# Optimization experiments

Hardware: AMD Instinct MI355X
Metric: run time of the kernel (lower is better)

Reference implementation:

```python
import jax, jax.numpy as jnp
import numpy as np

N, E, B = 200000, 1600000, 4096
IN_FEATS, H, R, NB = 64, 32, 8, 2


def _params(key):
    ks = jax.random.split(key, 20)
    p = {}
    dims = [(IN_FEATS, H), (H, H), (H, H), (H, H)]
    i = 0
    for l, (di, do) in enumerate(dims):
        p[f'basis{l}'] = jax.random.normal(ks[i], (NB, di, do), jnp.float32) * 0.1; i += 1
        p[f'comp{l}'] = jax.random.normal(ks[i], (R, NB), jnp.float32) * 0.1; i += 1
        p[f'wself{l}'] = jax.random.normal(ks[i], (di, do), jnp.float32) * 0.1; i += 1
        p[f'bias{l}'] = jnp.zeros((do,), jnp.float32); i += 1
    p['lin1_w'] = jax.random.normal(ks[i], (2 * 4 * H, 1), jnp.float32) * 0.05; i += 1
    p['lin1_b'] = jnp.zeros((1,), jnp.float32)
    return p


def setup_inputs() -> dict:
    key = jax.random.key(0)
    k = jax.random.split(key, 8)
    inp = {
        'x': jax.random.normal(k[0], (N, IN_FEATS), jnp.float32),
        'src': jax.random.randint(k[1], (E,), 0, N, jnp.int32),
        'dst': jax.random.randint(k[2], (E,), 0, N, jnp.int32),
        'etype': jax.random.randint(k[3], (E,), 0, R, jnp.int32),
        'user_idx': jax.random.randint(k[4], (B,), 0, N, jnp.int32),
        'item_idx': jax.random.randint(k[5], (B,), 0, N, jnp.int32),
    }
    inp.update(_params(k[6]))
    return inp


def _rel_graph_conv(x, src, dst, etype, basis, comp, wself, bias):
    # basis decomposition: W_r = sum_b comp[r,b] * basis[b]
    # compute per-node per-basis transform first (cheap: small NB), then mix per edge
    hb = jnp.einsum('ni,bio->nbo', x, basis)            # [N, NB, out]
    msg = jnp.einsum('eb,ebo->eo', comp[etype], hb[src])  # [E, out]
    agg = jax.ops.segment_sum(msg, dst, num_segments=x.shape[0])
    return agg + x @ wself + bias


def reference(x, src, dst, etype, user_idx, item_idx,
              basis0, comp0, wself0, bias0,
              basis1, comp1, wself1, bias1,
              basis2, comp2, wself2, bias2,
              basis3, comp3, wself3, bias3,
              lin1_w, lin1_b):
    states = []
    h = x
    for (ba, co, ws, bi) in ((basis0, comp0, wself0, bias0),
                             (basis1, comp1, wself1, bias1),
                             (basis2, comp2, wself2, bias2),
                             (basis3, comp3, wself3, bias3)):
        h = jnp.tanh(_rel_graph_conv(h, src, dst, etype, ba, co, ws, bi))
        states.append(h)
    cat = jnp.concatenate(states, axis=1)               # [N, 128]
    pair = jnp.concatenate([cat[user_idx], cat[item_idx]], axis=1)  # [B, 256]
    out = jax.nn.sigmoid(pair @ lin1_w + lin1_b)        # [B, 1]
    return out[:, 0]  # multiply_by == 1
```

## Files before the change

kernel.cpp:

```cpp
#include <hip/hip_runtime.h>
#include <hip/hip_bf16.h>


#define SRC_MASK 0x3FFFFu
#define BUK_SH 9
#define BUK_W 512

typedef __attribute__((ext_vector_type(8))) short bf16x8;
typedef __attribute__((ext_vector_type(4))) float f32x4;

__device__ inline unsigned int f2bf(float f) {
    unsigned int u = __float_as_uint(f);
    return (u + 0x7FFFu + ((u >> 16) & 1u)) >> 16;
}

__device__ inline float fast_tanh(float x) {
    float xc = fminf(fmaxf(x, -15.f), 15.f);
    float e = __expf(2.f * xc);
    return (e - 1.f) * __builtin_amdgcn_rcpf(e + 1.f);
}

__device__ inline void block_exscan(int* a, int M, int* wsum ) {
    const int t = threadIdx.x;
    const int q = M >> 2;
    int s0 = 0, s1 = 0, s2 = 0, s3 = 0, s = 0;
    if (t < q) {
        s0 = a[4 * t]; s1 = a[4 * t + 1]; s2 = a[4 * t + 2]; s3 = a[4 * t + 3];
        s = s0 + s1 + s2 + s3;
    }
    int lane = t & 63, wid = t >> 6;
    int val = s;
    for (int d = 1; d < 64; d <<= 1) {
        int u = __shfl_up(val, d, 64);
        if (lane >= d) val += u;
    }
    if (lane == 63) wsum[wid] = val;
    __syncthreads();
    int woff = 0;
    for (int w = 0; w < wid; ++w) woff += wsum[w];
    val += woff;
    int base = val - s;
    __syncthreads();
    if (t < q) {
        a[4 * t]     = base;
        a[4 * t + 1] = base + s0;
        a[4 * t + 2] = base + s0 + s1;
        a[4 * t + 3] = base + s0 + s1 + s2;
    }
    __syncthreads();
}

__global__ __launch_bounds__(256) void k_buk_count(const int* __restrict__ dst,
                                                   int* __restrict__ gBukCnt, int E) {
    __shared__ int hist[1024];
    const int t = threadIdx.x;
    for (int f = t; f < 1024; f += 256) hist[f] = 0;
    __syncthreads();
    int e0 = blockIdx.x * 2048;
    for (int k = 0; k < 8; ++k) {
        int e = e0 + k * 256 + t;
        if (e < E) atomicAdd(&hist[dst[e] >> BUK_SH], 1);
    }
    __syncthreads();
    for (int f = t; f < 1024; f += 256) {
        int c = hist[f];
        if (c) atomicAdd(&gBukCnt[f], c);
    }
}

__global__ void k_buk_scan(const int* __restrict__ gBukCnt, int* __restrict__ bukOff,
                           int nb) {
    __shared__ int lds[1024];
    int tid = threadIdx.x;
    int v = (tid < nb) ? gBukCnt[tid] : 0;
    lds[tid] = v;
    __syncthreads();
    for (int d = 1; d < 1024; d <<= 1) {
        int u = (tid >= d) ? lds[tid - d] : 0;
        __syncthreads();
        lds[tid] += u;
        __syncthreads();
    }
    if (tid < nb) bukOff[tid] = lds[tid] - v;
    if (tid == nb - 1) bukOff[nb] = lds[tid];
}

__global__ __launch_bounds__(256) void k_binscatter(
    const int* __restrict__ src, const int* __restrict__ dst,
    const int* __restrict__ etype, const int* __restrict__ bukOff,
    int* __restrict__ gBukCur, unsigned int* __restrict__ binned,
    int E, int NBUK)
{
    __shared__ int hist[1024];
    __shared__ int offs[1024];
    __shared__ int cur[1024];
    __shared__ int gb[1024];
    __shared__ int wsum[4];
    __shared__ unsigned int stage[2048];
    __shared__ unsigned short stageB[2048];
    const int t = threadIdx.x;
    for (int f = t; f < 1024; f += 256) { hist[f] = 0; cur[f] = 0; }
    __syncthreads();

    const int e0 = blockIdx.x * 2048;
    const int cntTot = min(2048, E - e0);
    unsigned int pk[8];
    int bk[8];
#pragma unroll
    for (int k = 0; k < 8; ++k) {
        int e = e0 + k * 256 + t;
        if (e < E) {
            int d = dst[e];
            bk[k] = d >> BUK_SH;
            pk[k] = (unsigned int)src[e]
                  | ((unsigned int)etype[e] << 29)
                  | ((unsigned int)(d & (BUK_W - 1)) << 20);
            atomicAdd(&hist[bk[k]], 1);
        } else bk[k] = -1;
    }
    __syncthreads();
    for (int f = t; f < 1024; f += 256) offs[f] = hist[f];
    __syncthreads();
    block_exscan(offs, 1024, wsum);
#pragma unroll
    for (int k = 0; k < 8; ++k) {
        if (bk[k] >= 0) {
            int pos = offs[bk[k]] + atomicAdd(&cur[bk[k]], 1);
            stage[pos] = pk[k];
            stageB[pos] = (unsigned short)bk[k];
        }
    }
    for (int f = t; f < NBUK; f += 256) {
        int c = hist[f];
        if (c > 0) gb[f] = bukOff[f] + atomicAdd(&gBukCur[f], c);
    }
    __syncthreads();
    for (int k = t; k < cntTot; k += 256) {
        int b = stageB[k];
        binned[(size_t)gb[b] + (size_t)(k - offs[b])] = stage[k];
    }
}

__global__ __launch_bounds__(256) void k_bucket_finalize(
    const unsigned int* __restrict__ binned, const int* __restrict__ bukOff,
    int* __restrict__ rowptr, unsigned int* __restrict__ epack, int N, int E)
{
    __shared__ int nhist[512];
    __shared__ int ncur[512];
    __shared__ int wsum[4];
    const int t = threadIdx.x;
    const int b = blockIdx.x;
    for (int f = t; f < 512; f += 256) { nhist[f] = 0; ncur[f] = 0; }
    __syncthreads();
    const int k0 = bukOff[b], k1 = bukOff[b + 1];
    for (int k = k0 + t; k < k1; k += 256)
        atomicAdd(&nhist[(binned[k] >> 20) & (BUK_W - 1)], 1);
    __syncthreads();
    block_exscan(nhist, 512, wsum);
    for (int f = t; f < 512; f += 256) {
        int node = (b << BUK_SH) + f;
        if (node < N) rowptr[node] = k0 + nhist[f];
    }
    if (b == 0 && t == 0) rowptr[N] = E;
    for (int k = k0 + t; k < k1; k += 256) {
        unsigned int v = binned[k];
        int dl = (v >> 20) & (BUK_W - 1);
        int pos = k0 + nhist[dl] + atomicAdd(&ncur[dl], 1);
        epack[pos] = v & 0xE003FFFFu;
    }
}

template<int DI>
__global__ __launch_bounds__(256) void k_transform3(
    const float* __restrict__ xin, int in_stride,
    const float* __restrict__ basis, const float* __restrict__ wself,
    const float* __restrict__ bias,
    unsigned int* __restrict__ hb2, float* __restrict__ selfout, int n)
{
    constexpr int ROWB = DI * 2;
    constexpr int SMASK = (ROWB / 16) - 1;
    constexpr int C4 = DI / 4;
    __shared__ unsigned short xs[64 * DI];
    __shared__ unsigned short bt[96 * DI];
    const int t = threadIdx.x;

    auto swz = [](int row, int byteInRow) -> int {
        int slot = (byteInRow >> 4) ^ ((row ^ (row >> 2)) & SMASK);
        return row * ROWB + (slot << 4) + (byteInRow & 15);
    };

    for (int f = t; f < 96 * C4; f += 256) {
        int k4 = f / 96;
        int o  = f - k4 * 96;
        const float* sp = (o < 64) ? (basis + (size_t)(o >> 5) * DI * 32 + (o & 31))
                                   : (wself + (o - 64));
        int k = 4 * k4;
        ushort4 pv;
        pv.x = (unsigned short)f2bf(sp[(size_t)(k + 0) * 32]);
        pv.y = (unsigned short)f2bf(sp[(size_t)(k + 1) * 32]);
        pv.z = (unsigned short)f2bf(sp[(size_t)(k + 2) * 32]);
        pv.w = (unsigned short)f2bf(sp[(size_t)(k + 3) * 32]);
        *(ushort4*)((char*)bt + swz(o, k * 2)) = pv;
    }

    const int node0 = blockIdx.x * 64;
    for (int f = t; f < 64 * C4; f += 256) {
        int nloc = f / C4, k4 = f - nloc * C4;
        int node = node0 + nloc;
        float4 v = make_float4(0.f, 0.f, 0.f, 0.f);
        if (node < n) v = *(const float4*)(xin + (size_t)node * in_stride + 4 * k4);
        ushort4 pv;
        pv.x = (unsigned short)f2bf(v.x);
        pv.y = (unsigned short)f2bf(v.y);
        pv.z = (unsigned short)f2bf(v.z);
        pv.w = (unsigned short)f2bf(v.w);
        *(ushort4*)((char*)xs + swz(nloc, 8 * k4)) = pv;
    }
    __syncthreads();

    const int w = t >> 6;
    const int l = t & 63;
    const int lr = l & 15;
    const int lg = l >> 4;

    f32x4 c[6];
#pragma unroll
    for (int i = 0; i < 6; ++i) c[i] = (f32x4){0.f, 0.f, 0.f, 0.f};

#pragma unroll
    for (int ks = 0; ks < DI / 32; ++ks) {
        const int kb = ks * 64 + lg * 16;
        bf16x8 a = *(const bf16x8*)((char*)xs + swz(w * 16 + lr, kb));
#pragma unroll
        for (int tt = 0; tt < 6; ++tt) {
            bf16x8 b = *(const bf16x8*)((char*)bt + swz(tt * 16 + lr, kb));
            c[tt] = __builtin_amdgcn_mfma_f32_16x16x32_bf16(a, b, c[tt], 0, 0, 0);
        }
    }

    const float bia0 = bias[lr];
    const float bia1 = bias[16 + lr];
#pragma unroll
    for (int r = 0; r < 4; ++r) {
        int node = node0 + w * 16 + lg * 4 + r;
        if (node < n) {
            hb2[(size_t)node * 32 + lr]      = f2bf(c[0][r]) | (f2bf(c[2][r]) << 16);
            hb2[(size_t)node * 32 + 16 + lr] = f2bf(c[1][r]) | (f2bf(c[3][r]) << 16);
            selfout[(size_t)node * 128 + lr]      = c[4][r] + bia0;
            selfout[(size_t)node * 128 + 16 + lr] = c[5][r] + bia1;
        }
    }
}

__global__ __launch_bounds__(256) void k_aggregate(
    const unsigned int* __restrict__ hb2,
    const unsigned int* __restrict__ epack,
    const int* __restrict__ rowptr,
    const float* __restrict__ comp,
    float* __restrict__ cat_l,
    int n)
{
    __shared__ unsigned int cw[8];
    if (threadIdx.x < 8)
        cw[threadIdx.x] = f2bf(comp[threadIdx.x * 2 + 0])
                        | (f2bf(comp[threadIdx.x * 2 + 1]) << 16);
    __syncthreads();
    int t = blockIdx.x * 256 + threadIdx.x;
    int node = t >> 3;
    int oj = t & 7;
    if (node >= n) return;
    float* cp = cat_l + (size_t)node * 128 + 4 * oj;
    float4 acc = *(float4*)cp;
    const int k0 = rowptr[node], k1 = rowptr[node + 1];
    const unsigned gbase = (unsigned)oj * 16u;
    for (int k = k0; k < k1; k += 8) {
        unsigned int pp[8];
        uint4 hh[8];
#pragma unroll
        for (int j = 0; j < 8; ++j)
            pp[j] = epack[min(k + j, k1 - 1)];
#pragma unroll
        for (int j = 0; j < 8; ++j) {
            unsigned boff = (pp[j] & SRC_MASK) * 128u + gbase;
            hh[j] = *(const uint4*)((const char*)hb2 + boff);
        }
#pragma unroll
        for (int j = 0; j < 8; ++j) {
            bool valid = (k + j) < k1;
            unsigned w = cw[pp[j] >> 29];
            float w0 = __uint_as_float(w << 16);
            float w1 = __uint_as_float(w & 0xFFFF0000u);
            unsigned hx = valid ? hh[j].x : 0u;
            unsigned hy = valid ? hh[j].y : 0u;
            unsigned hz = valid ? hh[j].z : 0u;
            unsigned hw = valid ? hh[j].w : 0u;
            acc.x = fmaf(w0, __uint_as_float(hx << 16), acc.x);
            acc.x = fmaf(w1, __uint_as_float(hx & 0xFFFF0000u), acc.x);
            acc.y = fmaf(w0, __uint_as_float(hy << 16), acc.y);
            acc.y = fmaf(w1, __uint_as_float(hy & 0xFFFF0000u), acc.y);
            acc.z = fmaf(w0, __uint_as_float(hz << 16), acc.z);
            acc.z = fmaf(w1, __uint_as_float(hz & 0xFFFF0000u), acc.z);
            acc.w = fmaf(w0, __uint_as_float(hw << 16), acc.w);
            acc.w = fmaf(w1, __uint_as_float(hw & 0xFFFF0000u), acc.w);
        }
    }
    float4 r;
    r.x = fast_tanh(acc.x);
    r.y = fast_tanh(acc.y);
    r.z = fast_tanh(acc.z);
    r.w = fast_tanh(acc.w);
    *(float4*)cp = r;
}

__global__ void k_head(const float* __restrict__ cat, const int* __restrict__ uidx,
                       const int* __restrict__ iidx, const float* __restrict__ w,
                       const float* __restrict__ b, float* __restrict__ out, int B) {
    int p = blockIdx.x;
    if (p >= B) return;
    int lane = threadIdx.x;
    const float* cu = cat + (size_t)uidx[p] * 128;
    const float* ci = cat + (size_t)iidx[p] * 128;
    float s = 0.f;
    s = fmaf(cu[lane], w[lane], s);
    s = fmaf(cu[lane + 64], w[lane + 64], s);
    s = fmaf(ci[lane], w[lane + 128], s);
    s = fmaf(ci[lane + 64], w[lane + 192], s);
    for (int d = 32; d > 0; d >>= 1) s += __shfl_down(s, d, 64);
    if (lane == 0) out[p] = 1.f / (1.f + expf(-(s + b[0])));
}

extern "C" void kernel_launch(void* const* d_in, const int* in_sizes, int n_in,
                              void* d_out, int out_size, void* d_ws, size_t ws_size,
                              hipStream_t stream) {
    const float* x      = (const float*)d_in[0];
    const int*   src    = (const int*)d_in[1];
    const int*   dst    = (const int*)d_in[2];
    const int*   etype  = (const int*)d_in[3];
    const int*   uidx   = (const int*)d_in[4];
    const int*   iidx   = (const int*)d_in[5];
    const float* lin1_w = (const float*)d_in[22];
    const float* lin1_b = (const float*)d_in[23];

    const int N = in_sizes[0] / 64;
    const int E = in_sizes[1];
    const int B = in_sizes[4];
    const int NBUK = (N + BUK_W - 1) >> BUK_SH;

    char* p = (char*)d_ws;
    auto alloc = [&](size_t bytes) -> void* {
        void* r = (void*)p;
        p += (bytes + 255) & ~(size_t)255;
        return r;
    };
    unsigned int* hb2     = (unsigned int*)alloc((size_t)N * 32 * sizeof(unsigned int));
    float*        cat     = (float*)alloc((size_t)N * 128 * sizeof(float));
    int*          rowptr  = (int*)alloc((size_t)(N + 1) * sizeof(int));
    unsigned int* epack   = (unsigned int*)alloc((size_t)E * sizeof(unsigned int));
    unsigned int* binned  = (unsigned int*)alloc((size_t)E * sizeof(unsigned int));
    int*          gBukCnt = (int*)alloc(1024 * sizeof(int));
    int*          gBukCur = (int*)alloc(1024 * sizeof(int));
    int*          bukOff  = (int*)alloc(1025 * sizeof(int));

    hipMemsetAsync(gBukCnt, 0, 2048 * sizeof(int), stream);
    int ebGrid = (E + 2047) / 2048;
    k_buk_count<<<ebGrid, 256, 0, stream>>>(dst, gBukCnt, E);
    k_buk_scan<<<1, 1024, 0, stream>>>(gBukCnt, bukOff, NBUK);
    k_binscatter<<<ebGrid, 256, 0, stream>>>(src, dst, etype, bukOff, gBukCur,
                                             binned, E, NBUK);
    k_bucket_finalize<<<NBUK, 256, 0, stream>>>(binned, bukOff, rowptr, epack, N, E);

    int tr_grid = (N + 63) / 64;
    int agg_grid = (N * 8 + 255) / 256;
    for (int l = 0; l < 4; ++l) {
        const float* xin   = (l == 0) ? x : (cat + (size_t)(l - 1) * 32);
        int in_stride      = (l == 0) ? 64 : 128;
        const float* basis = (const float*)d_in[6 + l * 4];
        const float* comp  = (const float*)d_in[7 + l * 4];
        const float* wself = (const float*)d_in[8 + l * 4];
        const float* bias  = (const float*)d_in[9 + l * 4];
        if (l == 0)
            k_transform3<64><<<tr_grid, 256, 0, stream>>>(xin, in_stride, basis, wself,
                                                          bias, hb2, cat + (size_t)l * 32, N);
        else
            k_transform3<32><<<tr_grid, 256, 0, stream>>>(xin, in_stride, basis, wself,
                                                          bias, hb2, cat + (size_t)l * 32, N);
        k_aggregate<<<agg_grid, 256, 0, stream>>>(hb2, epack, rowptr, comp,
                                                  cat + (size_t)l * 32, N);
    }

    k_head<<<B, 64, 0, stream>>>(cat, uidx, iidx, lin1_w, lin1_b, (float*)d_out, B);
}
```

Measured before the change: 291.6 us.

## Sort nodes by in-degree to balance aggregate wavefront work

Adds a counting sort of nodes by in-degree (histogram, scan, scatter kernels) and has the aggregate kernel process nodes in that order. Nodes in the same wavefront then have similar edge counts, which cuts divergence in the per-node edge loop. The cost is three extra kernels per call, one more level of indirection, and scattered rather than sequential writes to the output rows, which hurts locality. With random uniform graphs the degree spread is small (Poisson around 8), so the balancing gain may be limited.

```diff
diff --git a/kernel.cpp b/kernel.cpp
--- a/kernel.cpp
+++ b/kernel.cpp
@@ -170,6 +170,70 @@
     }
 }
 
+__global__ __launch_bounds__(256) void k_deg_hist(const int* __restrict__ rowptr,
+                                                  int* __restrict__ gDegCnt, int N) {
+    __shared__ int h[64];
+    const int t = threadIdx.x;
+    if (t < 64) h[t] = 0;
+    __syncthreads();
+    int i0 = blockIdx.x * 2048;
+    for (int k = 0; k < 8; ++k) {
+        int i = i0 + k * 256 + t;
+        if (i < N) atomicAdd(&h[min(rowptr[i + 1] - rowptr[i], 63)], 1);
+    }
+    __syncthreads();
+    if (t < 64) {
+        int c = h[t];
+        if (c) atomicAdd(&gDegCnt[t], c);
+    }
+}
+
+__global__ void k_deg_scan(const int* __restrict__ gDegCnt, int* __restrict__ degOff) {
+    __shared__ int lds[64];
+    int t = threadIdx.x;
+    lds[t] = gDegCnt[t];
+    __syncthreads();
+    if (t == 0) {
+        int s = 0;
+        for (int i = 0; i < 64; ++i) { int c = lds[i]; lds[i] = s; s += c; }
+    }
+    __syncthreads();
+    degOff[t] = lds[t];
+}
+
+__global__ __launch_bounds__(256) void k_deg_scatter(const int* __restrict__ rowptr,
+                                                     const int* __restrict__ degOff,
+                                                     int* __restrict__ gDegCur,
+                                                     int* __restrict__ nodeOrder, int N) {
+    __shared__ int h[64], base[64], cur[64];
+    const int t = threadIdx.x;
+    if (t < 64) { h[t] = 0; cur[t] = 0; }
+    __syncthreads();
+    int i0 = blockIdx.x * 2048;
+    int dg[8];
+#pragma unroll
+    for (int k = 0; k < 8; ++k) {
+        int i = i0 + k * 256 + t;
+        if (i < N) {
+            dg[k] = min(rowptr[i + 1] - rowptr[i], 63);
+            atomicAdd(&h[dg[k]], 1);
+        } else dg[k] = -1;
+    }
+    __syncthreads();
+    if (t < 64) {
+        int c = h[t];
+        if (c) base[t] = degOff[t] + atomicAdd(&gDegCur[t], c);
+    }
+    __syncthreads();
+#pragma unroll
+    for (int k = 0; k < 8; ++k) {
+        if (dg[k] >= 0) {
+            int r = atomicAdd(&cur[dg[k]], 1);
+            nodeOrder[base[dg[k]] + r] = i0 + k * 256 + t;
+        }
+    }
+}
+
 template<int DI>
 __global__ __launch_bounds__(256) void k_transform3(
     const float* __restrict__ xin, int in_stride,
@@ -256,6 +320,7 @@
     const unsigned int* __restrict__ hb2,
     const unsigned int* __restrict__ epack,
     const int* __restrict__ rowptr,
+    const int* __restrict__ nodeOrder,
     const float* __restrict__ comp,
     float* __restrict__ cat_l,
     int n)
@@ -266,9 +331,10 @@
                         | (f2bf(comp[threadIdx.x * 2 + 1]) << 16);
     __syncthreads();
     int t = blockIdx.x * 256 + threadIdx.x;
-    int node = t >> 3;
+    int idx = t >> 3;
     int oj = t & 7;
-    if (node >= n) return;
+    if (idx >= n) return;
+    int node = nodeOrder[idx];
     float* cp = cat_l + (size_t)node * 128 + 4 * oj;
     float4 acc = *(float4*)cp;
     const int k0 = rowptr[node], k1 = rowptr[node + 1];
@@ -352,22 +418,32 @@
         p += (bytes + 255) & ~(size_t)255;
         return r;
     };
-    unsigned int* hb2     = (unsigned int*)alloc((size_t)N * 32 * sizeof(unsigned int));
-    float*        cat     = (float*)alloc((size_t)N * 128 * sizeof(float));
-    int*          rowptr  = (int*)alloc((size_t)(N + 1) * sizeof(int));
-    unsigned int* epack   = (unsigned int*)alloc((size_t)E * sizeof(unsigned int));
-    unsigned int* binned  = (unsigned int*)alloc((size_t)E * sizeof(unsigned int));
-    int*          gBukCnt = (int*)alloc(1024 * sizeof(int));
-    int*          gBukCur = (int*)alloc(1024 * sizeof(int));
-    int*          bukOff  = (int*)alloc(1025 * sizeof(int));
+    unsigned int* hb2      = (unsigned int*)alloc((size_t)N * 32 * sizeof(unsigned int));
+    float*        cat      = (float*)alloc((size_t)N * 128 * sizeof(float));
+    int*          rowptr   = (int*)alloc((size_t)(N + 1) * sizeof(int));
+    unsigned int* epack    = (unsigned int*)alloc((size_t)E * sizeof(unsigned int));
+    unsigned int* binned   = (unsigned int*)alloc((size_t)E * sizeof(unsigned int));
+    int*          nodeOrder= (int*)alloc((size_t)N * sizeof(int));
+    int*          gBukCnt  = (int*)alloc(1024 * sizeof(int));
+    int*          gBukCur  = (int*)alloc(1024 * sizeof(int));
+    int*          bukOff   = (int*)alloc(1025 * sizeof(int));
+    int*          gDegCnt  = (int*)alloc(64 * sizeof(int));
+    int*          gDegCur  = (int*)alloc(64 * sizeof(int));
+    int*          degOff   = (int*)alloc(64 * sizeof(int));
 
     hipMemsetAsync(gBukCnt, 0, 2048 * sizeof(int), stream);
+    hipMemsetAsync(gDegCnt, 0, 128 * sizeof(int), stream);
     int ebGrid = (E + 2047) / 2048;
+    int nbGrid = (N + 2047) / 2048;
     k_buk_count<<<ebGrid, 256, 0, stream>>>(dst, gBukCnt, E);
     k_buk_scan<<<1, 1024, 0, stream>>>(gBukCnt, bukOff, NBUK);
     k_binscatter<<<ebGrid, 256, 0, stream>>>(src, dst, etype, bukOff, gBukCur,
                                              binned, E, NBUK);
     k_bucket_finalize<<<NBUK, 256, 0, stream>>>(binned, bukOff, rowptr, epack, N, E);
+
+    k_deg_hist<<<nbGrid, 256, 0, stream>>>(rowptr, gDegCnt, N);
+    k_deg_scan<<<1, 64, 0, stream>>>(gDegCnt, degOff);
+    k_deg_scatter<<<nbGrid, 256, 0, stream>>>(rowptr, degOff, gDegCur, nodeOrder, N);
 
     int tr_grid = (N + 63) / 64;
     int agg_grid = (N * 8 + 255) / 256;
@@ -384,7 +460,7 @@
         else
             k_transform3<32><<<tr_grid, 256, 0, stream>>>(xin, in_stride, basis, wself,
                                                           bias, hb2, cat + (size_t)l * 32, N);
-        k_aggregate<<<agg_grid, 256, 0, stream>>>(hb2, epack, rowptr, comp,
+        k_aggregate<<<agg_grid, 256, 0, stream>>>(hb2, epack, rowptr, nodeOrder, comp,
                                                   cat + (size_t)l * 32, N);
     }
 
```

Measured after the change: 318.1 us. +9.1%, slower.
